# Performance work log

Measured on AMD Instinct MI355X. Metric: run time of the kernel, lower is better.

## Reference

```python
import jax, jax.numpy as jnp
import numpy as np

B, T, D, H = 8, 4096, 1024, 16
DK = D // H
CHUNK = 64
E, TOPK, MULT, CAPF = 8, 2, 4, 1.25
HID = D * MULT
N = B * T
CAPACITY = int(CAPF * (N / E))  # 5120


def setup_inputs() -> dict:
    key = jax.random.key(0)
    ks = jax.random.split(key, 16)
    s = 0.02
    r = lambda k, shape: jax.random.normal(k, shape, jnp.float32) * s
    return {
        "x": jax.random.normal(ks[0], (B, T, D), jnp.float32),
        "norm1_scale": jnp.ones((D,), jnp.float32),
        "norm2_scale": jnp.ones((D,), jnp.float32),
        "Wq": r(ks[1], (D, D)), "bq": jnp.zeros((D,), jnp.float32),
        "Wk": r(ks[2], (D, D)), "bk": jnp.zeros((D,), jnp.float32),
        "Wv": r(ks[3], (D, D)), "bv": jnp.zeros((D,), jnp.float32),
        "Wg": r(ks[4], (D, D)), "bg": jnp.zeros((D,), jnp.float32),
        "Wo": r(ks[5], (D, D)), "bo": jnp.zeros((D,), jnp.float32),
        "router_W": r(ks[6], (D, E)), "router_b": jnp.zeros((E,), jnp.float32),
        "W1": r(ks[7], (E, D, HID)), "b1": jnp.zeros((E, HID), jnp.float32),
        "W2": r(ks[8], (E, HID, D)), "b2": jnp.zeros((E, D), jnp.float32),
    }


def rmsnorm(x, scale):
    # torch: x / (||x|| / sqrt(d)) * scale == x * rsqrt(mean(x^2)) * scale (no eps)
    return x / jnp.sqrt(jnp.mean(x * x, axis=-1, keepdims=True)) * scale


def apply_rope(x):
    # x: (B, H, T, DK); non-interleaved half-rotation as in source
    half = x.shape[-1] // 2
    t = x.shape[2]
    inv = 1.0 / (10000.0 ** (jnp.arange(half, dtype=jnp.float32) / half))
    ang = jnp.arange(t, dtype=jnp.float32)[:, None] * inv[None, :]  # (T, half)
    sin, cos = jnp.sin(ang)[None, None], jnp.cos(ang)[None, None]
    x1, x2 = x[..., :half], x[..., half:]
    return jnp.concatenate([x1 * cos - x2 * sin, x1 * sin + x2 * cos], axis=-1)


def phi(x):
    return jax.nn.elu(x) + 1.0


def attention(x, Wq, bq, Wk, bk, Wv, bv, Wg, bg, Wo, bo):
    b, t, c = x.shape
    heads = lambda y: y.reshape(b, t, H, DK).transpose(0, 2, 1, 3)  # (B,H,T,DK)
    q = phi(apply_rope(heads(x @ Wq + bq)))
    k = phi(apply_rope(heads(x @ Wk + bk)))
    v = heads(x @ Wv + bv)
    g = heads(jax.nn.sigmoid(x @ Wg + bg))
    nc = t // CHUNK
    to_chunks = lambda y: y.reshape(b, H, nc, CHUNK, DK).transpose(2, 0, 1, 3, 4)
    qs, ks_, vs, gs = map(to_chunks, (q, k, v, g))  # (nc,B,H,chunk,DK)
    S0 = jnp.zeros((b, H, DK, DK), x.dtype)
    Z0 = jnp.zeros((b, H, DK), x.dtype)

    def step(carry, inp):
        S, Z = carry
        qc, kc, vc, gc = inp
        S = S + jnp.einsum('bhtd,bhte->bhde', kc, vc)
        Z = Z + kc.sum(axis=2)
        num = jnp.einsum('bhtd,bhde->bhte', qc, S)
        den = jnp.einsum('bhtd,bhd->bht', qc, Z)[..., None] + 1e-6
        return (S, Z), gc * (num / den)

    _, outs = jax.lax.scan(step, (S0, Z0), (qs, ks_, vs, gs))  # (nc,B,H,chunk,DK)
    out = outs.transpose(1, 2, 0, 3, 4).reshape(b, H, t, DK)
    out = out.transpose(0, 2, 1, 3).reshape(b, t, c)
    return out @ Wo + bo


def moe(x, router_W, router_b, W1, b1, W2, b2):
    b, t, c = x.shape
    n = b * t
    xf = x.reshape(n, c)
    probs = jax.nn.softmax(xf @ router_W + router_b, axis=-1)
    topk_probs, topk_idx = jax.lax.top_k(probs, TOPK)
    topk_probs = topk_probs / topk_probs.sum(axis=-1, keepdims=True)
    out = jnp.zeros_like(xf)
    load = []
    for eid in range(E):  # fixed small expert loop (matches source structure)
        mask = (topk_idx == eid).reshape(-1)  # row-major == torch.where order
        idx = jnp.nonzero(mask, size=CAPACITY, fill_value=n * TOPK)[0]
        valid = idx < n * TOPK
        idxc = jnp.minimum(idx, n * TOPK - 1)
        tok, choice = idxc // TOPK, idxc % TOPK
        h = jax.nn.gelu(xf[tok] @ W1[eid] + b1[eid], approximate=False) @ W2[eid] + b2[eid]
        gate = jnp.where(valid, topk_probs[tok, choice], 0.0)
        out = out.at[tok].add(gate[:, None] * h)  # invalid slots have gate==0
        load.append(jnp.minimum(mask.sum(), CAPACITY).astype(xf.dtype))
    load = jnp.stack(load)
    importance = probs.sum(axis=0)
    importance = importance / importance.sum()
    load = load / load.sum()
    aux = (importance * load).sum() * (E ** 2)
    return out.reshape(b, t, c), aux


def reference(x, norm1_scale, norm2_scale, Wq, bq, Wk, bk, Wv, bv, Wg, bg, Wo, bo,
              router_W, router_b, W1, b1, W2, b2):
    x = x + attention(rmsnorm(x, norm1_scale), Wq, bq, Wk, bk, Wv, bv, Wg, bg, Wo, bo)
    moe_out, aux = moe(rmsnorm(x, norm2_scale), router_W, router_b, W1, b1, W2, b2)
    return (x + moe_out, aux)
```

## Files before the change

kernel.cpp:

```cpp
#include <hip/hip_runtime.h>
#include <hip/hip_bf16.h>

#define NTOK 32768
#define TSEQ 4096
#define DM   1024
#define NHEAD 16
#define NEXP 8
#define CAPE 5120
#define HIDN 4096
#define GTOK 8192
#define KSPL 5120

#ifndef __has_builtin
#define __has_builtin(x) 0
#endif
#if __has_builtin(__builtin_amdgcn_global_load_lds)
#define HAVE_GLOAD 1
#else
#define HAVE_GLOAD 0
#endif

typedef __attribute__((ext_vector_type(8))) short bf16x8;
typedef __attribute__((ext_vector_type(4))) float f32x4;

// ... 135 lines not shown
    o.x = f2bf_bits(v.x * r * ns.x);
    o.y = f2bf_bits(v.y * r * ns.y);
    o.z = f2bf_bits(v.z * r * ns.z);
    o.w = f2bf_bits(v.w * r * ns.w);
    ((ushort4*)(xbf + (size_t)row * DM))[tid] = o;
}

#if HAVE_GLOAD
__device__ __forceinline__ void gload16(const __hip_bfloat16* g, __hip_bfloat16* l)
{
    __builtin_amdgcn_global_load_lds((const __attribute__((address_space(1))) unsigned int*)g,
                                     (__attribute__((address_space(3))) unsigned int*)l, 16, 0, 0);
}
#endif

struct ProjPack {
    const __hip_bfloat16* BT[4];
    const float* bias[4];
    float* C[4];
};

template<int NMAT, bool RESID>
__global__ __launch_bounds__(256) void k_gemm_proj(const __hip_bfloat16* __restrict__ A,
                                                   ProjPack P,
                                                   const float* __restrict__ resid)
{
    const int z = (NMAT == 4) ? blockIdx.z : 0;
    const __hip_bfloat16* BT = P.BT[z];
    const float* bias = P.bias[z];
    float* C = P.C[z];
    const int m0 = blockIdx.y * 128;
    const int n0 = blockIdx.x * 128;
    const int tid = threadIdx.x;
    __shared__ alignas(16) __hip_bfloat16 As[128 * 32];
    __shared__ alignas(16) __hip_bfloat16 Bs[128 * 32];

    const int lane = tid & 63, wv = tid >> 6;
    const int lr = lane & 15, lgp = lane >> 4;
    const int wm = (wv >> 1) * 64, wn = (wv & 1) * 64;

#if HAVE_GLOAD
    const int rA0 = wv * 32 + (lane >> 2), rA1 = rA0 + 16;
    const int ch = lane & 3;
    const __hip_bfloat16* srcA0 = A + (size_t)(m0 + rA0) * 3072 + ((ch ^ (rA0 & 3)) * 8);
    const __hip_bfloat16* srcA1 = A + (size_t)(m0 + rA1) * 3072 + ((ch ^ (rA1 & 3)) * 8);
    const __hip_bfloat16* srcB0 = BT + (size_t)(n0 + rA0) * KSPL + ((ch ^ (rA0 & 3)) * 8);
    const __hip_bfloat16* srcB1 = BT + (size_t)(n0 + rA1) * KSPL + ((ch ^ (rA1 & 3)) * 8);
    __hip_bfloat16* ldsA0 = As + (size_t)(wv * 32) * 32;
    __hip_bfloat16* ldsA1 = As + (size_t)(wv * 32 + 16) * 32;
    __hip_bfloat16* ldsB0 = Bs + (size_t)(wv * 32) * 32;
    __hip_bfloat16* ldsB1 = Bs + (size_t)(wv * 32 + 16) * 32;
#else
    const int ar = tid >> 1, ac0 = (tid & 1) * 2;
    const __hip_bfloat16* Arow = A + (size_t)(m0 + ar) * 3072;
    const __hip_bfloat16* Brow = BT + (size_t)(n0 + ar) * KSPL;
#endif

    f32x4 acc[4][4];
#pragma unroll
    for (int i = 0; i < 4; ++i)
#pragma unroll
        for (int j = 0; j < 4; ++j) acc[i][j] = (f32x4){0.f, 0.f, 0.f, 0.f};

    int a_off[4], b_off[4];
#pragma unroll
    for (int i = 0; i < 4; ++i) {
        int mrow = wm + i * 16 + lr;
        a_off[i] = mrow * 32 + ((lgp ^ (mrow & 3)) * 8);
        int nrow = wn + i * 16 + lr;
        b_off[i] = nrow * 32 + ((lgp ^ (nrow & 3)) * 8);
    }

    for (int k0 = 0; k0 < KSPL; k0 += 32) {
        const int acol = (k0 < 3072) ? k0 : (k0 - 3072);
        __syncthreads();
#if HAVE_GLOAD
        gload16(srcA0 + acol, ldsA0);
        gload16(srcA1 + acol, ldsA1);
        gload16(srcB0 + k0, ldsB0);
        gload16(srcB1 + k0, ldsB1);
#else
        {
            uint4 av0 = *(const uint4*)(Arow + acol + ac0 * 8);
            uint4 av1 = *(const uint4*)(Arow + acol + ac0 * 8 + 8);
            uint4 bv0 = *(const uint4*)(Brow + k0 + ac0 * 8);
            uint4 bv1 = *(const uint4*)(Brow + k0 + ac0 * 8 + 8);
            *(uint4*)(As + ar * 32 + ((ac0    ) ^ (ar & 3)) * 8) = av0;
            *(uint4*)(As + ar * 32 + ((ac0 + 1) ^ (ar & 3)) * 8) = av1;
            *(uint4*)(Bs + ar * 32 + ((ac0    ) ^ (ar & 3)) * 8) = bv0;
            *(uint4*)(Bs + ar * 32 + ((ac0 + 1) ^ (ar & 3)) * 8) = bv1;
        }
#endif
        __syncthreads();
        bf16x8 af[4], bfr[4];
#pragma unroll
        for (int i = 0; i < 4; ++i) af[i] = *(const bf16x8*)(As + a_off[i]);
#pragma unroll
        for (int j = 0; j < 4; ++j) bfr[j] = *(const bf16x8*)(Bs + b_off[j]);
#pragma unroll
        for (int i = 0; i < 4; ++i)
#pragma unroll
            for (int j = 0; j < 4; ++j)
                acc[i][j] = __builtin_amdgcn_mfma_f32_16x16x32_bf16(af[i], bfr[j], acc[i][j], 0, 0, 0);
    }

#pragma unroll
    for (int i = 0; i < 4; ++i)
#pragma unroll
        for (int j = 0; j < 4; ++j) {
            const int col = n0 + wn + j * 16 + lr;
            const float bval = bias[col];
#pragma unroll
            for (int r = 0; r < 4; ++r) {
                const int rloc = wm + i * 16 + lgp * 4 + r;
                float v = acc[i][j][r] + bval;
                if (RESID) v += resid[(size_t)(m0 + rloc) * DM + col];
                C[(size_t)(m0 + rloc) * DM + col] = v;
            }
        }
}

__global__ __launch_bounds__(256) void k_scan_kv(float* KS, float* Vz,
                                                 const float* __restrict__ ct,
                                                 const float* __restrict__ st)
{
    const int c = blockIdx.x, bh = blockIdx.y;
    const int h = bh & 15, b = bh >> 4;
    const int tid = threadIdx.x;
    __shared__ float ks[64][68];
    __shared__ float vs[64][68];
    const size_t rowbase = ((size_t)b * TSEQ + c * 64) * DM + h * 64;
#pragma unroll
    for (int p = 0; p < 8; ++p) {
        int idx = p * 256 + tid;
        int t = idx >> 5, j = idx & 31;
        const size_t base = rowbase + (size_t)t * DM + j;
        float cn = ct[(c * 64 + t) * 32 + j];
        float sn = st[(c * 64 + t) * 32 + j];
        float k1 = KS[base], k2 = KS[base + 32];
        ks[t][j]      = phi_f(k1 * cn - k2 * sn);
        ks[t][j + 32] = phi_f(k1 * sn + k2 * cn);
    }
#pragma unroll
    for (int p = 0; p < 4; ++p) {
        int idx = p * 256 + tid;
        int t = idx >> 4, e4 = (idx & 15) * 4;
        *(float4*)&vs[t][e4] = *(const float4*)&Vz[rowbase + (size_t)t * DM + e4];
    }
    __syncthreads();
    const int e = tid & 63, dg = tid >> 6;
    float acc[16] = {};
    for (int t = 0; t < 64; ++t) {
        float vv = vs[t][e];
#pragma unroll
        for (int q = 0; q < 4; ++q) {
            float4 kq = *(const float4*)&ks[t][dg * 16 + q * 4];
            acc[q * 4 + 0] = fmaf(kq.x, vv, acc[q * 4 + 0]);
            acc[q * 4 + 1] = fmaf(kq.y, vv, acc[q * 4 + 1]);
            acc[q * 4 + 2] = fmaf(kq.z, vv, acc[q * 4 + 2]);
            acc[q * 4 + 3] = fmaf(kq.w, vv, acc[q * 4 + 3]);
        }
    }
#pragma unroll
    for (int i = 0; i < 16; ++i) {
        int d = dg * 16 + i;
        KS[rowbase + (size_t)d * DM + e] = acc[i];
    }
    if (tid < 64) {
        float z = 0.f;
        for (int t = 0; t < 64; ++t) z += ks[t][tid];
        Vz[rowbase + tid] = z;
    }
}

__global__ __launch_bounds__(256) void k_scan_prefix(float* S)
{
    const int sg = blockIdx.x, bh = blockIdx.y;
    const int h = bh & 15, b = bh >> 4;
    const int idx = sg * 256 + threadIdx.x;
    const int d = idx >> 6, e = idx & 63;
    const size_t base = (size_t)b * TSEQ * DM + h * 64 + (size_t)d * DM + e;
    float acc = 0.f;
    for (int c = 0; c < 64; ++c) {
        size_t p = base + (size_t)c * 64 * DM;
        acc += S[p];
        S[p] = acc;
    }
}

__global__ void k_zprefix(float* Vz)
{
    const int bh = blockIdx.x;
    const int h = bh & 15, b = bh >> 4;
    const int d = threadIdx.x;
    const size_t base = (size_t)b * TSEQ * DM + h * 64 + d;
    float acc = 0.f;
    for (int c = 0; c < 64; ++c) {
        size_t p = base + (size_t)c * 64 * DM;
        acc += Vz[p];
        Vz[p] = acc;
    }
}

__global__ __launch_bounds__(256) void k_scan_out(const float* __restrict__ Q,
                                                  const float* __restrict__ S,
                                                  const float* __restrict__ Zv,
                                                  float* GO,
                                                  const float* __restrict__ ct,
                                                  const float* __restrict__ st)
{
    const int c = blockIdx.x, bh = blockIdx.y;
    const int h = bh & 15, b = bh >> 4;
    const int tid = threadIdx.x;
    __shared__ float qs[64][69];
    __shared__ float Ss[64][68];
    __shared__ float den[64], Zl[64];
    const size_t rowbase = ((size_t)b * TSEQ + c * 64) * DM + h * 64;
#pragma unroll
    for (int p = 0; p < 8; ++p) {
        int idx = p * 256 + tid;
        int t = idx >> 5, j = idx & 31;
        const size_t base = rowbase + (size_t)t * DM + j;
        float cn = ct[(c * 64 + t) * 32 + j];
        float sn = st[(c * 64 + t) * 32 + j];
        float q1 = Q[base], q2 = Q[base + 32];
        qs[t][j]      = phi_f(q1 * cn - q2 * sn);
        qs[t][j + 32] = phi_f(q1 * sn + q2 * cn);
    }
#pragma unroll
    for (int p = 0; p < 4; ++p) {
        int idx = p * 256 + tid;
        int d = idx >> 4, e4 = (idx & 15) * 4;
        *(float4*)&Ss[d][e4] = *(const float4*)&S[rowbase + (size_t)d * DM + e4];
    }
    const int e = tid & 63, tg = tid >> 6;
    float greg[16];
#pragma unroll
    for (int i = 0; i < 16; ++i)
        greg[i] = GO[rowbase + (size_t)(tg * 16 + i) * DM + e];
    if (tid < 64) Zl[tid] = Zv[rowbase + tid];
    __syncthreads();
    if (tid < 64) {
        float dd = 0.f;
        for (int d = 0; d < 64; ++d) dd += qs[tid][d] * Zl[d];
        den[tid] = dd + 1e-6f;
    }
    __syncthreads();
    float acc[16] = {};
    for (int d = 0; d < 64; ++d) {
        float sv = Ss[d][e];
#pragma unroll
        for (int i = 0; i < 16; ++i)
            acc[i] = fmaf(qs[tg * 16 + i][d], sv, acc[i]);
    }
#pragma unroll
    for (int i = 0; i < 16; ++i) {
        int t = tg * 16 + i;
        float g = 1.f / (1.f + expf(-greg[i]));
        GO[rowbase + (size_t)t * DM + e] = g * acc[i] / den[t];
    }
}

__global__ __launch_bounds__(256) void k_router(const float* __restrict__ X2,
                                                const float* __restrict__ rn2,
                                                const float* __restrict__ ns2,
                                                const float* __restrict__ rW,
                                                const float* __restrict__ rb,
                                                int* __restrict__ route_e,
                                                float* __restrict__ route_g,
                                                float* __restrict__ probs)
{
    const int tok = blockIdx.x * 4 + (threadIdx.x >> 6);
    const int lane = threadIdx.x & 63;
    const float* xr = X2 + (size_t)tok * DM;
    const float rn = rn2[tok];
    float lg[8] = {};
    for (int d = lane; d < DM; d += 64) {
        float xv = xr[d] * rn * ns2[d];
        const float4* w4 = (const float4*)(rW + (size_t)d * 8);
        float4 w0 = w4[0], w1 = w4[1];
        lg[0] += xv * w0.x; lg[1] += xv * w0.y; lg[2] += xv * w0.z; lg[3] += xv * w0.w;
        lg[4] += xv * w1.x; lg[5] += xv * w1.y; lg[6] += xv * w1.z; lg[7] += xv * w1.w;
    }
#pragma unroll
    for (int e = 0; e < 8; ++e)
        for (int off = 32; off; off >>= 1) lg[e] += __shfl_xor(lg[e], off);
    if (lane == 0) {
        float pe[8]; float mx = -1e30f, s = 0.f;
#pragma unroll
        for (int e = 0; e < 8; ++e) { lg[e] += rb[e]; mx = fmaxf(mx, lg[e]); }
#pragma unroll
        for (int e = 0; e < 8; ++e) { pe[e] = expf(lg[e] - mx); s += pe[e]; }
#pragma unroll
        for (int e = 0; e < 8; ++e) { pe[e] /= s; probs[(size_t)tok * 8 + e] = pe[e]; }
        int i1 = 0; float p1 = pe[0];
#pragma unroll
        for (int e = 1; e < 8; ++e) if (pe[e] > p1) { p1 = pe[e]; i1 = e; }
        int i2 = -1; float p2 = -1.f;
#pragma unroll
        for (int e = 0; e < 8; ++e) if (e != i1 && pe[e] > p2) { p2 = pe[e]; i2 = e; }
        const float gsum = p1 + p2;
        route_e[tok * 2] = i1; route_e[tok * 2 + 1] = i2;
        route_g[tok * 2] = p1 / gsum; route_g[tok * 2 + 1] = p2 / gsum;
    }
}

__global__ __launch_bounds__(256) void k_count(const int* __restrict__ route_e, int* __restrict__ bcnt)
{
    __shared__ int c[8];
    const int tid = threadIdx.x;
    if (tid < 8) c[tid] = 0;
    __syncthreads();
    atomicAdd(&c[route_e[blockIdx.x * 256 + tid]], 1);
    __syncthreads();
    if (tid < 8) bcnt[blockIdx.x * 8 + tid] = c[tid];
}

__global__ void k_scan_blocks(const int* __restrict__ bcnt, int* __restrict__ bbase, int* __restrict__ ctot)
{
    const int e = threadIdx.x;
    if (e < 8) {
        int run = 0;
        for (int b = 0; b < 256; ++b) { bbase[b * 8 + e] = run; run += bcnt[b * 8 + e]; }
        ctot[e] = run;
    }
}

__global__ __launch_bounds__(256) void k_place(const int* __restrict__ route_e,
                                               const float* __restrict__ route_g,
                                               const int* __restrict__ bbase,
                                               int* __restrict__ tokslot,
                                               float* __restrict__ gateslot)
{
    const int tid = threadIdx.x;
    const int a = blockIdx.x * 256 + tid;
    const int e = route_e[a];
    __shared__ int se[256];
    se[tid] = e;
    __syncthreads();
    int rank = 0;
    for (int j = 0; j < tid; ++j) rank += (se[j] == e) ? 1 : 0;
    const int slot = bbase[blockIdx.x * 8 + e] + rank;
    if (slot < CAPE) {
        tokslot[e * CAPE + slot] = a >> 1;
        gateslot[e * CAPE + slot] = route_g[a];
    }
}

__global__ __launch_bounds__(256) void k_aux(const float* __restrict__ probs,
                                             const int* __restrict__ ctot,
                                             float* __restrict__ out_aux)
{
    const int tid = threadIdx.x;
    float part[8] = {};
    for (int i = tid; i < NTOK; i += 256) {
        const float* p = probs + (size_t)i * 8;
#pragma unroll
        for (int e = 0; e < 8; ++e) part[e] += p[e];
    }
    __shared__ float red[256];
    __shared__ float accs[8];
    for (int e = 0; e < 8; ++e) {
        red[tid] = part[e];
        __syncthreads();
        for (int s = 128; s; s >>= 1) { if (tid < s) red[tid] += red[tid + s]; __syncthreads(); }
        if (tid == 0) accs[e] = red[0];
        __syncthreads();
    }
    if (tid == 0) {
        float isum = 0.f, lsum = 0.f, l[8];
        for (int e = 0; e < 8; ++e) isum += accs[e];
        for (int e = 0; e < 8; ++e) { l[e] = fminf((float)ctot[e], (float)CAPE); lsum += l[e]; }
        float aux = 0.f;
        for (int e = 0; e < 8; ++e) aux += (accs[e] / isum) * (l[e] / lsum);
        out_aux[0] = aux * 64.f;
    }
}

__global__ void k_transpose_bf16(const float* __restrict__ src, __hip_bfloat16* __restrict__ dst,
                                 int K_, int N_)
{
    __shared__ float t_[32][33];
    const int z = blockIdx.z;
    const float* s = src + (size_t)z * K_ * N_;
    __hip_bfloat16* d = dst + (size_t)z * K_ * N_;
    const int n0 = blockIdx.x * 32, k0 = blockIdx.y * 32;
    const int c = threadIdx.x, r0 = threadIdx.y;
#pragma unroll
    for (int i = 0; i < 4; ++i) { int r = r0 + i * 8; t_[r][c] = s[(size_t)(k0 + r) * N_ + n0 + c]; }
    __syncthreads();
#pragma unroll
    for (int i = 0; i < 4; ++i) { int r = r0 + i * 8; d[(size_t)(n0 + r) * K_ + k0 + c] = __float2bfloat16(t_[c][r]); }
}

template<int MODE>
__global__ __launch_bounds__(256) void k_gemm_bf16(const __hip_bfloat16* __restrict__ A,
                                                   const __hip_bfloat16* __restrict__ BT,
                                                   const float* __restrict__ bias,
                                                   __hip_bfloat16* __restrict__ Hout,
                                                   float* __restrict__ Fout,
                                                   const int* __restrict__ tokslot,
                                                   const float* __restrict__ gateslot,
                                                   int K, int Nout, int e0)
{
    const int le = blockIdx.z;
    const int e = e0 + le;
    const int m0 = blockIdx.y * 128;
    const int n0 = blockIdx.x * 128;
    const int tid = threadIdx.x;
    __shared__ alignas(16) __hip_bfloat16 As[128 * 32];
    __shared__ alignas(16) __hip_bfloat16 Bs[128 * 32];
    __shared__ int s_tok[128];
    __shared__ float s_gate[128];
    if (tid < 128) {
        s_tok[tid] = tokslot[e * CAPE + m0 + tid];
        s_gate[tid] = gateslot[e * CAPE + m0 + tid];
    }
    __syncthreads();

    const int lane = tid & 63, wv = tid >> 6;
    const int lr = lane & 15, lgp = lane >> 4;
    const int wm = (wv >> 1) * 64, wn = (wv & 1) * 64;

#if HAVE_GLOAD
    const int rA0 = wv * 32 + (lane >> 2), rA1 = rA0 + 16;
    const int ch = lane & 3;
    const __hip_bfloat16 *srcA0, *srcA1;
    if (MODE == 0) {
        srcA0 = A + (size_t)s_tok[rA0] * K + ((ch ^ (rA0 & 3)) * 8);
        srcA1 = A + (size_t)s_tok[rA1] * K + ((ch ^ (rA1 & 3)) * 8);
    } else {
        srcA0 = A + ((size_t)le * CAPE + m0 + rA0) * K + ((ch ^ (rA0 & 3)) * 8);
        srcA1 = A + ((size_t)le * CAPE + m0 + rA1) * K + ((ch ^ (rA1 & 3)) * 8);
    }
    const __hip_bfloat16* srcB0 = BT + ((size_t)e * Nout + n0 + rA0) * K + ((ch ^ (rA0 & 3)) * 8);
    const __hip_bfloat16* srcB1 = BT + ((size_t)e * Nout + n0 + rA1) * K + ((ch ^ (rA1 & 3)) * 8);
    __hip_bfloat16* ldsA0 = As + (size_t)(wv * 32) * 32;
    __hip_bfloat16* ldsA1 = As + (size_t)(wv * 32 + 16) * 32;
    __hip_bfloat16* ldsB0 = Bs + (size_t)(wv * 32) * 32;
    __hip_bfloat16* ldsB1 = Bs + (size_t)(wv * 32 + 16) * 32;
#else
    const int ar = tid >> 1, ac0 = (tid & 1) * 2;
    const __hip_bfloat16* Arow;
    if (MODE == 0) Arow = A + (size_t)s_tok[ar] * K;
    else           Arow = A + ((size_t)le * CAPE + m0 + ar) * K;
    const __hip_bfloat16* Brow = BT + ((size_t)e * Nout + n0 + ar) * K;
#endif

    f32x4 acc[4][4];
#pragma unroll
    for (int i = 0; i < 4; ++i)
#pragma unroll
        for (int j = 0; j < 4; ++j) acc[i][j] = (f32x4){0.f, 0.f, 0.f, 0.f};

    int a_off[4], b_off[4];
#pragma unroll
    for (int i = 0; i < 4; ++i) {
        int mrow = wm + i * 16 + lr;
        a_off[i] = mrow * 32 + ((lgp ^ (mrow & 3)) * 8);
        int nrow = wn + i * 16 + lr;
        b_off[i] = nrow * 32 + ((lgp ^ (nrow & 3)) * 8);
    }

    for (int k0 = 0; k0 < K; k0 += 32) {
        __syncthreads();
#if HAVE_GLOAD
        gload16(srcA0 + k0, ldsA0);
        gload16(srcA1 + k0, ldsA1);
        gload16(srcB0 + k0, ldsB0);
        gload16(srcB1 + k0, ldsB1);
#else
        {
            uint4 av0 = *(const uint4*)(Arow + k0 + ac0 * 8);
            uint4 av1 = *(const uint4*)(Arow + k0 + ac0 * 8 + 8);
            uint4 bv0 = *(const uint4*)(Brow + k0 + ac0 * 8);
            uint4 bv1 = *(const uint4*)(Brow + k0 + ac0 * 8 + 8);
            *(uint4*)(As + ar * 32 + ((ac0    ) ^ (ar & 3)) * 8) = av0;
            *(uint4*)(As + ar * 32 + ((ac0 + 1) ^ (ar & 3)) * 8) = av1;
            *(uint4*)(Bs + ar * 32 + ((ac0    ) ^ (ar & 3)) * 8) = bv0;
            *(uint4*)(Bs + ar * 32 + ((ac0 + 1) ^ (ar & 3)) * 8) = bv1;
        }
#endif
        __syncthreads();
        bf16x8 af[4], bfr[4];
#pragma unroll
        for (int i = 0; i < 4; ++i) af[i] = *(const bf16x8*)(As + a_off[i]);
#pragma unroll
        for (int j = 0; j < 4; ++j) bfr[j] = *(const bf16x8*)(Bs + b_off[j]);
#pragma unroll
        for (int i = 0; i < 4; ++i)
#pragma unroll
            for (int j = 0; j < 4; ++j)
                acc[i][j] = __builtin_amdgcn_mfma_f32_16x16x32_bf16(af[i], bfr[j], acc[i][j], 0, 0, 0);
    }

#pragma unroll
    for (int i = 0; i < 4; ++i)
#pragma unroll
        for (int j = 0; j < 4; ++j) {
            const int col = n0 + wn + j * 16 + lr;
            const float bval = bias[(size_t)e * Nout + col];
#pragma unroll
            for (int r = 0; r < 4; ++r) {
                const int rloc = wm + i * 16 + lgp * 4 + r;
                float v = acc[i][j][r] + bval;
                if (MODE == 0) {
                    v = 0.5f * v * (1.f + erff(v * 0.70710678118654752f));
                    Hout[((size_t)le * CAPE + m0 + rloc) * Nout + col] = __float2bfloat16(v);
                } else {
                    const float g = s_gate[rloc];
                    if (g != 0.f) atomicAdd(&Fout[(size_t)s_tok[rloc] * DM + col], v * g);
                }
            }
        }
}

extern "C" void kernel_launch(void* const* d_in, const int* in_sizes, int n_in,
                              void* d_out, int out_size, void* d_ws, size_t ws_size,
                              hipStream_t stream)
{
    (void)in_sizes; (void)n_in; (void)out_size;
    const float* x   = (const float*)d_in[0];
    const float* ns1 = (const float*)d_in[1];
    const float* ns2 = (const float*)d_in[2];
    const float* Wq  = (const float*)d_in[3];
    const float* bq  = (const float*)d_in[4];
    const float* Wk  = (const float*)d_in[5];
    const float* bk  = (const float*)d_in[6];
    const float* Wv  = (const float*)d_in[7];
// ... 64 lines not shown
        const float* xg = x + tok0 * DM;
        float* vg = out + tok0 * DM;

        k_rms_split<true><<<GTOK, 256, 0, stream>>>(xg, ns1, Xs);

        ProjPack P;
        P.BT[0] = WST;                     P.bias[0] = bq; P.C[0] = qg;
        P.BT[1] = WST + (size_t)DM * KSPL; P.bias[1] = bk; P.C[1] = kg;
        P.BT[2] = WST + 2ull * DM * KSPL;  P.bias[2] = bg; P.C[2] = gg;
        P.BT[3] = WST + 3ull * DM * KSPL;  P.bias[3] = bv; P.C[3] = vg;
        k_gemm_proj<4, false><<<dim3(8, GTOK / 128, 4), 256, 0, stream>>>(Xs, P, nullptr);

        k_scan_kv<<<dim3(64, 32), 256, 0, stream>>>(kg, vg, rope_ct, rope_st);
        k_scan_prefix<<<dim3(16, 32), 256, 0, stream>>>(kg);
        k_zprefix<<<32, 64, 0, stream>>>(vg);
        k_scan_out<<<dim3(64, 32), 256, 0, stream>>>(qg, kg, vg, gg, rope_ct, rope_st);

        k_rms_split<false><<<GTOK, 256, 0, stream>>>(gg, nullptr, Xs);

        ProjPack P2;
        P2.BT[0] = WST + 4ull * DM * KSPL; P2.bias[0] = bo; P2.C[0] = vg;
        P2.BT[1] = P2.BT[2] = P2.BT[3] = P2.BT[0];
        P2.bias[1] = P2.bias[2] = P2.bias[3] = bo;
        P2.C[1] = P2.C[2] = P2.C[3] = vg;
        k_gemm_proj<1, true><<<dim3(8, GTOK / 128, 1), 256, 0, stream>>>(Xs, P2, xg);

        k_rmsnorm_stats<<<GTOK, 256, 0, stream>>>(vg, rn2 + tok0, ns2, xn2bf + tok0 * DM);
    }

    k_router<<<NTOK / 4, 256, 0, stream>>>(out, rn2, ns2, rW, rb, route_e, route_g, probs);

    k_count<<<256, 256, 0, stream>>>(route_e, bcnt);
    k_scan_blocks<<<1, 64, 0, stream>>>(bcnt, bbase, ctot);
// ... 18 lines not shown
```

Before: 4.618 ms.

## Double-buffer LDS in GEMM kernels and fuse bf16 split into scan output

Both the projection GEMM and the expert GEMM now use two LDS buffers per operand. The next K-slice is prefetched into the spare buffer while MFMAs run on the current one, leaving one barrier per iteration instead of two. The scan output kernel now writes the three-way bf16 split directly into the GEMM input buffer, which removes the separate k_rms_split pass over the gated output. The cost is double the LDS per block, which may lower occupancy.

```diff
diff --git a/kernel.cpp b/kernel.cpp
--- a/kernel.cpp
+++ b/kernel.cpp
@@ -173,6 +173,7 @@
 }
 #endif
 
+
 struct ProjPack {
     const __hip_bfloat16* BT[4];
     const float* bias[4];
@@ -191,8 +192,8 @@
     const int m0 = blockIdx.y * 128;
     const int n0 = blockIdx.x * 128;
     const int tid = threadIdx.x;
-    __shared__ alignas(16) __hip_bfloat16 As[128 * 32];
-    __shared__ alignas(16) __hip_bfloat16 Bs[128 * 32];
+    __shared__ alignas(16) __hip_bfloat16 As[2][128 * 32];
+    __shared__ alignas(16) __hip_bfloat16 Bs[2][128 * 32];
 
     const int lane = tid & 63, wv = tid >> 6;
     const int lr = lane & 15, lgp = lane >> 4;
@@ -205,10 +206,8 @@
     const __hip_bfloat16* srcA1 = A + (size_t)(m0 + rA1) * 3072 + ((ch ^ (rA1 & 3)) * 8);
     const __hip_bfloat16* srcB0 = BT + (size_t)(n0 + rA0) * KSPL + ((ch ^ (rA0 & 3)) * 8);
     const __hip_bfloat16* srcB1 = BT + (size_t)(n0 + rA1) * KSPL + ((ch ^ (rA1 & 3)) * 8);
-    __hip_bfloat16* ldsA0 = As + (size_t)(wv * 32) * 32;
-    __hip_bfloat16* ldsA1 = As + (size_t)(wv * 32 + 16) * 32;
-    __hip_bfloat16* ldsB0 = Bs + (size_t)(wv * 32) * 32;
-    __hip_bfloat16* ldsB1 = Bs + (size_t)(wv * 32 + 16) * 32;
+    const int ldsO0 = (wv * 32) * 32;
+    const int ldsO1 = (wv * 32 + 16) * 32;
 #else
     const int ar = tid >> 1, ac0 = (tid & 1) * 2;
     const __hip_bfloat16* Arow = A + (size_t)(m0 + ar) * 3072;
@@ -230,37 +229,58 @@
         b_off[i] = nrow * 32 + ((lgp ^ (nrow & 3)) * 8);
     }
 
+#if HAVE_GLOAD
+    gload16(srcA0, &As[0][ldsO0]);
+    gload16(srcA1, &As[0][ldsO1]);
+    gload16(srcB0, &Bs[0][ldsO0]);
+    gload16(srcB1, &Bs[0][ldsO1]);
+#else
+    {
+        uint4 av0 = *(const uint4*)(Arow + ac0 * 8);
+        uint4 av1 = *(const uint4*)(Arow + ac0 * 8 + 8);
+        uint4 bv0 = *(const uint4*)(Brow + ac0 * 8);
+        uint4 bv1 = *(const uint4*)(Brow + ac0 * 8 + 8);
+        *(uint4*)(&As[0][0] + ar * 32 + ((ac0    ) ^ (ar & 3)) * 8) = av0;
+        *(uint4*)(&As[0][0] + ar * 32 + ((ac0 + 1) ^ (ar & 3)) * 8) = av1;
+        *(uint4*)(&Bs[0][0] + ar * 32 + ((ac0    ) ^ (ar & 3)) * 8) = bv0;
+        *(uint4*)(&Bs[0][0] + ar * 32 + ((ac0 + 1) ^ (ar & 3)) * 8) = bv1;
+    }
+#endif
+    __syncthreads();
+
+    int cur = 0;
     for (int k0 = 0; k0 < KSPL; k0 += 32) {
-        const int acol = (k0 < 3072) ? k0 : (k0 - 3072);
-        __syncthreads();
+        if (k0 + 32 < KSPL) {
+            const int kn = k0 + 32;
+            const int acoln = (kn < 3072) ? kn : (kn - 3072);
 #if HAVE_GLOAD
-        gload16(srcA0 + acol, ldsA0);
-        gload16(srcA1 + acol, ldsA1);
-        gload16(srcB0 + k0, ldsB0);
-        gload16(srcB1 + k0, ldsB1);
+            gload16(srcA0 + acoln, &As[cur ^ 1][ldsO0]);
+            gload16(srcA1 + acoln, &As[cur ^ 1][ldsO1]);
+            gload16(srcB0 + kn, &Bs[cur ^ 1][ldsO0]);
+            gload16(srcB1 + kn, &Bs[cur ^ 1][ldsO1]);
 #else
-        {
-            uint4 av0 = *(const uint4*)(Arow + acol + ac0 * 8);
-            uint4 av1 = *(const uint4*)(Arow + acol + ac0 * 8 + 8);
-            uint4 bv0 = *(const uint4*)(Brow + k0 + ac0 * 8);
-            uint4 bv1 = *(const uint4*)(Brow + k0 + ac0 * 8 + 8);
-            *(uint4*)(As + ar * 32 + ((ac0    ) ^ (ar & 3)) * 8) = av0;
-            *(uint4*)(As + ar * 32 + ((ac0 + 1) ^ (ar & 3)) * 8) = av1;
-            *(uint4*)(Bs + ar * 32 + ((ac0    ) ^ (ar & 3)) * 8) = bv0;
-            *(uint4*)(Bs + ar * 32 + ((ac0 + 1) ^ (ar & 3)) * 8) = bv1;
+            uint4 av0 = *(const uint4*)(Arow + acoln + ac0 * 8);
+            uint4 av1 = *(const uint4*)(Arow + acoln + ac0 * 8 + 8);
+            uint4 bv0 = *(const uint4*)(Brow + kn + ac0 * 8);
+            uint4 bv1 = *(const uint4*)(Brow + kn + ac0 * 8 + 8);
+            *(uint4*)(&As[cur ^ 1][0] + ar * 32 + ((ac0    ) ^ (ar & 3)) * 8) = av0;
+            *(uint4*)(&As[cur ^ 1][0] + ar * 32 + ((ac0 + 1) ^ (ar & 3)) * 8) = av1;
+            *(uint4*)(&Bs[cur ^ 1][0] + ar * 32 + ((ac0    ) ^ (ar & 3)) * 8) = bv0;
+            *(uint4*)(&Bs[cur ^ 1][0] + ar * 32 + ((ac0 + 1) ^ (ar & 3)) * 8) = bv1;
+#endif
         }
-#endif
-        __syncthreads();
         bf16x8 af[4], bfr[4];
 #pragma unroll
-        for (int i = 0; i < 4; ++i) af[i] = *(const bf16x8*)(As + a_off[i]);
-#pragma unroll
-        for (int j = 0; j < 4; ++j) bfr[j] = *(const bf16x8*)(Bs + b_off[j]);
+        for (int i = 0; i < 4; ++i) af[i] = *(const bf16x8*)(&As[cur][0] + a_off[i]);
+#pragma unroll
+        for (int j = 0; j < 4; ++j) bfr[j] = *(const bf16x8*)(&Bs[cur][0] + b_off[j]);
 #pragma unroll
         for (int i = 0; i < 4; ++i)
 #pragma unroll
             for (int j = 0; j < 4; ++j)
                 acc[i][j] = __builtin_amdgcn_mfma_f32_16x16x32_bf16(af[i], bfr[j], acc[i][j], 0, 0, 0);
+        __syncthreads();
+        cur ^= 1;
     }
 
 #pragma unroll
@@ -277,279 +297,6 @@
                 C[(size_t)(m0 + rloc) * DM + col] = v;
             }
         }
-}
-
-__global__ __launch_bounds__(256) void k_scan_kv(float* KS, float* Vz,
-                                                 const float* __restrict__ ct,
-                                                 const float* __restrict__ st)
-{
-    const int c = blockIdx.x, bh = blockIdx.y;
-    const int h = bh & 15, b = bh >> 4;
-    const int tid = threadIdx.x;
-    __shared__ float ks[64][68];
-    __shared__ float vs[64][68];
-    const size_t rowbase = ((size_t)b * TSEQ + c * 64) * DM + h * 64;
-#pragma unroll
-    for (int p = 0; p < 8; ++p) {
-        int idx = p * 256 + tid;
-        int t = idx >> 5, j = idx & 31;
-        const size_t base = rowbase + (size_t)t * DM + j;
-        float cn = ct[(c * 64 + t) * 32 + j];
-        float sn = st[(c * 64 + t) * 32 + j];
-        float k1 = KS[base], k2 = KS[base + 32];
-        ks[t][j]      = phi_f(k1 * cn - k2 * sn);
-        ks[t][j + 32] = phi_f(k1 * sn + k2 * cn);
-    }
-#pragma unroll
-    for (int p = 0; p < 4; ++p) {
-        int idx = p * 256 + tid;
-        int t = idx >> 4, e4 = (idx & 15) * 4;
-        *(float4*)&vs[t][e4] = *(const float4*)&Vz[rowbase + (size_t)t * DM + e4];
-    }
-    __syncthreads();
-    const int e = tid & 63, dg = tid >> 6;
-    float acc[16] = {};
-    for (int t = 0; t < 64; ++t) {
-        float vv = vs[t][e];
-#pragma unroll
-        for (int q = 0; q < 4; ++q) {
-            float4 kq = *(const float4*)&ks[t][dg * 16 + q * 4];
-            acc[q * 4 + 0] = fmaf(kq.x, vv, acc[q * 4 + 0]);
-            acc[q * 4 + 1] = fmaf(kq.y, vv, acc[q * 4 + 1]);
-            acc[q * 4 + 2] = fmaf(kq.z, vv, acc[q * 4 + 2]);
-            acc[q * 4 + 3] = fmaf(kq.w, vv, acc[q * 4 + 3]);
-        }
-    }
-#pragma unroll
-    for (int i = 0; i < 16; ++i) {
-        int d = dg * 16 + i;
-        KS[rowbase + (size_t)d * DM + e] = acc[i];
-    }
-    if (tid < 64) {
-        float z = 0.f;
-        for (int t = 0; t < 64; ++t) z += ks[t][tid];
-        Vz[rowbase + tid] = z;
-    }
-}
-
-__global__ __launch_bounds__(256) void k_scan_prefix(float* S)
-{
-    const int sg = blockIdx.x, bh = blockIdx.y;
-    const int h = bh & 15, b = bh >> 4;
-    const int idx = sg * 256 + threadIdx.x;
-    const int d = idx >> 6, e = idx & 63;
-    const size_t base = (size_t)b * TSEQ * DM + h * 64 + (size_t)d * DM + e;
-    float acc = 0.f;
-    for (int c = 0; c < 64; ++c) {
-        size_t p = base + (size_t)c * 64 * DM;
-        acc += S[p];
-        S[p] = acc;
-    }
-}
-
-__global__ void k_zprefix(float* Vz)
-{
-    const int bh = blockIdx.x;
-    const int h = bh & 15, b = bh >> 4;
-    const int d = threadIdx.x;
-    const size_t base = (size_t)b * TSEQ * DM + h * 64 + d;
-    float acc = 0.f;
-    for (int c = 0; c < 64; ++c) {
-        size_t p = base + (size_t)c * 64 * DM;
-        acc += Vz[p];
-        Vz[p] = acc;
-    }
-}
-
-__global__ __launch_bounds__(256) void k_scan_out(const float* __restrict__ Q,
-                                                  const float* __restrict__ S,
-                                                  const float* __restrict__ Zv,
-                                                  float* GO,
-                                                  const float* __restrict__ ct,
-                                                  const float* __restrict__ st)
-{
-    const int c = blockIdx.x, bh = blockIdx.y;
-    const int h = bh & 15, b = bh >> 4;
-    const int tid = threadIdx.x;
-    __shared__ float qs[64][69];
-    __shared__ float Ss[64][68];
-    __shared__ float den[64], Zl[64];
-    const size_t rowbase = ((size_t)b * TSEQ + c * 64) * DM + h * 64;
-#pragma unroll
-    for (int p = 0; p < 8; ++p) {
-        int idx = p * 256 + tid;
-        int t = idx >> 5, j = idx & 31;
-        const size_t base = rowbase + (size_t)t * DM + j;
-        float cn = ct[(c * 64 + t) * 32 + j];
-        float sn = st[(c * 64 + t) * 32 + j];
-        float q1 = Q[base], q2 = Q[base + 32];
-        qs[t][j]      = phi_f(q1 * cn - q2 * sn);
-        qs[t][j + 32] = phi_f(q1 * sn + q2 * cn);
-    }
-#pragma unroll
-    for (int p = 0; p < 4; ++p) {
-        int idx = p * 256 + tid;
-        int d = idx >> 4, e4 = (idx & 15) * 4;
-        *(float4*)&Ss[d][e4] = *(const float4*)&S[rowbase + (size_t)d * DM + e4];
-    }
-    const int e = tid & 63, tg = tid >> 6;
-    float greg[16];
-#pragma unroll
-    for (int i = 0; i < 16; ++i)
-        greg[i] = GO[rowbase + (size_t)(tg * 16 + i) * DM + e];
-    if (tid < 64) Zl[tid] = Zv[rowbase + tid];
-    __syncthreads();
-    if (tid < 64) {
-        float dd = 0.f;
-        for (int d = 0; d < 64; ++d) dd += qs[tid][d] * Zl[d];
-        den[tid] = dd + 1e-6f;
-    }
-    __syncthreads();
-    float acc[16] = {};
-    for (int d = 0; d < 64; ++d) {
-        float sv = Ss[d][e];
-#pragma unroll
-        for (int i = 0; i < 16; ++i)
-            acc[i] = fmaf(qs[tg * 16 + i][d], sv, acc[i]);
-    }
-#pragma unroll
-    for (int i = 0; i < 16; ++i) {
-        int t = tg * 16 + i;
-        float g = 1.f / (1.f + expf(-greg[i]));
-        GO[rowbase + (size_t)t * DM + e] = g * acc[i] / den[t];
-    }
-}
-
-__global__ __launch_bounds__(256) void k_router(const float* __restrict__ X2,
-                                                const float* __restrict__ rn2,
-                                                const float* __restrict__ ns2,
-                                                const float* __restrict__ rW,
-                                                const float* __restrict__ rb,
-                                                int* __restrict__ route_e,
-                                                float* __restrict__ route_g,
-                                                float* __restrict__ probs)
-{
-    const int tok = blockIdx.x * 4 + (threadIdx.x >> 6);
-    const int lane = threadIdx.x & 63;
-    const float* xr = X2 + (size_t)tok * DM;
-    const float rn = rn2[tok];
-    float lg[8] = {};
-    for (int d = lane; d < DM; d += 64) {
-        float xv = xr[d] * rn * ns2[d];
-        const float4* w4 = (const float4*)(rW + (size_t)d * 8);
-        float4 w0 = w4[0], w1 = w4[1];
-        lg[0] += xv * w0.x; lg[1] += xv * w0.y; lg[2] += xv * w0.z; lg[3] += xv * w0.w;
-        lg[4] += xv * w1.x; lg[5] += xv * w1.y; lg[6] += xv * w1.z; lg[7] += xv * w1.w;
-    }
-#pragma unroll
-    for (int e = 0; e < 8; ++e)
-        for (int off = 32; off; off >>= 1) lg[e] += __shfl_xor(lg[e], off);
-    if (lane == 0) {
-        float pe[8]; float mx = -1e30f, s = 0.f;
-#pragma unroll
-        for (int e = 0; e < 8; ++e) { lg[e] += rb[e]; mx = fmaxf(mx, lg[e]); }
-#pragma unroll
-        for (int e = 0; e < 8; ++e) { pe[e] = expf(lg[e] - mx); s += pe[e]; }
-#pragma unroll
-        for (int e = 0; e < 8; ++e) { pe[e] /= s; probs[(size_t)tok * 8 + e] = pe[e]; }
-        int i1 = 0; float p1 = pe[0];
-#pragma unroll
-        for (int e = 1; e < 8; ++e) if (pe[e] > p1) { p1 = pe[e]; i1 = e; }
-        int i2 = -1; float p2 = -1.f;
-#pragma unroll
-        for (int e = 0; e < 8; ++e) if (e != i1 && pe[e] > p2) { p2 = pe[e]; i2 = e; }
-        const float gsum = p1 + p2;
-        route_e[tok * 2] = i1; route_e[tok * 2 + 1] = i2;
-        route_g[tok * 2] = p1 / gsum; route_g[tok * 2 + 1] = p2 / gsum;
-    }
-}
-
-__global__ __launch_bounds__(256) void k_count(const int* __restrict__ route_e, int* __restrict__ bcnt)
-{
-    __shared__ int c[8];
-    const int tid = threadIdx.x;
-    if (tid < 8) c[tid] = 0;
-    __syncthreads();
-    atomicAdd(&c[route_e[blockIdx.x * 256 + tid]], 1);
-    __syncthreads();
-    if (tid < 8) bcnt[blockIdx.x * 8 + tid] = c[tid];
-}
-
-__global__ void k_scan_blocks(const int* __restrict__ bcnt, int* __restrict__ bbase, int* __restrict__ ctot)
-{
-    const int e = threadIdx.x;
-    if (e < 8) {
-        int run = 0;
-        for (int b = 0; b < 256; ++b) { bbase[b * 8 + e] = run; run += bcnt[b * 8 + e]; }
-        ctot[e] = run;
-    }
-}
-
-__global__ __launch_bounds__(256) void k_place(const int* __restrict__ route_e,
-                                               const float* __restrict__ route_g,
-                                               const int* __restrict__ bbase,
-                                               int* __restrict__ tokslot,
-                                               float* __restrict__ gateslot)
-{
-    const int tid = threadIdx.x;
-    const int a = blockIdx.x * 256 + tid;
-    const int e = route_e[a];
-    __shared__ int se[256];
-    se[tid] = e;
-    __syncthreads();
-    int rank = 0;
-    for (int j = 0; j < tid; ++j) rank += (se[j] == e) ? 1 : 0;
-    const int slot = bbase[blockIdx.x * 8 + e] + rank;
-    if (slot < CAPE) {
-        tokslot[e * CAPE + slot] = a >> 1;
-        gateslot[e * CAPE + slot] = route_g[a];
-    }
-}
-
-__global__ __launch_bounds__(256) void k_aux(const float* __restrict__ probs,
-                                             const int* __restrict__ ctot,
-                                             float* __restrict__ out_aux)
-{
-    const int tid = threadIdx.x;
-    float part[8] = {};
-    for (int i = tid; i < NTOK; i += 256) {
-        const float* p = probs + (size_t)i * 8;
-#pragma unroll
-        for (int e = 0; e < 8; ++e) part[e] += p[e];
-    }
-    __shared__ float red[256];
-    __shared__ float accs[8];
-    for (int e = 0; e < 8; ++e) {
-        red[tid] = part[e];
-        __syncthreads();
-        for (int s = 128; s; s >>= 1) { if (tid < s) red[tid] += red[tid + s]; __syncthreads(); }
-        if (tid == 0) accs[e] = red[0];
-        __syncthreads();
-    }
-    if (tid == 0) {
-        float isum = 0.f, lsum = 0.f, l[8];
-        for (int e = 0; e < 8; ++e) isum += accs[e];
-        for (int e = 0; e < 8; ++e) { l[e] = fminf((float)ctot[e], (float)CAPE); lsum += l[e]; }
-        float aux = 0.f;
-        for (int e = 0; e < 8; ++e) aux += (accs[e] / isum) * (l[e] / lsum);
-        out_aux[0] = aux * 64.f;
-    }
-}
-
-__global__ void k_transpose_bf16(const float* __restrict__ src, __hip_bfloat16* __restrict__ dst,
-                                 int K_, int N_)
-{
-    __shared__ float t_[32][33];
-    const int z = blockIdx.z;
-    const float* s = src + (size_t)z * K_ * N_;
-    __hip_bfloat16* d = dst + (size_t)z * K_ * N_;
-    const int n0 = blockIdx.x * 32, k0 = blockIdx.y * 32;
-    const int c = threadIdx.x, r0 = threadIdx.y;
-#pragma unroll
-    for (int i = 0; i < 4; ++i) { int r = r0 + i * 8; t_[r][c] = s[(size_t)(k0 + r) * N_ + n0 + c]; }
-    __syncthreads();
-#pragma unroll
-    for (int i = 0; i < 4; ++i) { int r = r0 + i * 8; d[(size_t)(n0 + r) * K_ + k0 + c] = __float2bfloat16(t_[c][r]); }
 }
 
 template<int MODE>
@@ -567,8 +314,8 @@
     const int m0 = blockIdx.y * 128;
     const int n0 = blockIdx.x * 128;
     const int tid = threadIdx.x;
-    __shared__ alignas(16) __hip_bfloat16 As[128 * 32];
-    __shared__ alignas(16) __hip_bfloat16 Bs[128 * 32];
+    __shared__ alignas(16) __hip_bfloat16 As[2][128 * 32];
+    __shared__ alignas(16) __hip_bfloat16 Bs[2][128 * 32];
     __shared__ int s_tok[128];
     __shared__ float s_gate[128];
     if (tid < 128) {
@@ -594,10 +341,8 @@
     }
     const __hip_bfloat16* srcB0 = BT + ((size_t)e * Nout + n0 + rA0) * K + ((ch ^ (rA0 & 3)) * 8);
     const __hip_bfloat16* srcB1 = BT + ((size_t)e * Nout + n0 + rA1) * K + ((ch ^ (rA1 & 3)) * 8);
-    __hip_bfloat16* ldsA0 = As + (size_t)(wv * 32) * 32;
-    __hip_bfloat16* ldsA1 = As + (size_t)(wv * 32 + 16) * 32;
-    __hip_bfloat16* ldsB0 = Bs + (size_t)(wv * 32) * 32;
-    __hip_bfloat16* ldsB1 = Bs + (size_t)(wv * 32 + 16) * 32;
+    const int ldsO0 = (wv * 32) * 32;
+    const int ldsO1 = (wv * 32 + 16) * 32;
 #else
     const int ar = tid >> 1, ac0 = (tid & 1) * 2;
     const __hip_bfloat16* Arow;
@@ -621,36 +366,57 @@
         b_off[i] = nrow * 32 + ((lgp ^ (nrow & 3)) * 8);
     }
 
+#if HAVE_GLOAD
+    gload16(srcA0, &As[0][ldsO0]);
+    gload16(srcA1, &As[0][ldsO1]);
+    gload16(srcB0, &Bs[0][ldsO0]);
+    gload16(srcB1, &Bs[0][ldsO1]);
+#else
+    {
+        uint4 av0 = *(const uint4*)(Arow + ac0 * 8);
+        uint4 av1 = *(const uint4*)(Arow + ac0 * 8 + 8);
+        uint4 bv0 = *(const uint4*)(Brow + ac0 * 8);
+        uint4 bv1 = *(const uint4*)(Brow + ac0 * 8 + 8);
+        *(uint4*)(&As[0][0] + ar * 32 + ((ac0    ) ^ (ar & 3)) * 8) = av0;
+        *(uint4*)(&As[0][0] + ar * 32 + ((ac0 + 1) ^ (ar & 3)) * 8) = av1;
+        *(uint4*)(&Bs[0][0] + ar * 32 + ((ac0    ) ^ (ar & 3)) * 8) = bv0;
+        *(uint4*)(&Bs[0][0] + ar * 32 + ((ac0 + 1) ^ (ar & 3)) * 8) = bv1;
+    }
+#endif
+    __syncthreads();
+
+    int cur = 0;
     for (int k0 = 0; k0 < K; k0 += 32) {
-        __syncthreads();
+        if (k0 + 32 < K) {
+            const int kn = k0 + 32;
 #if HAVE_GLOAD
-        gload16(srcA0 + k0, ldsA0);
-        gload16(srcA1 + k0, ldsA1);
-        gload16(srcB0 + k0, ldsB0);
-        gload16(srcB1 + k0, ldsB1);
+            gload16(srcA0 + kn, &As[cur ^ 1][ldsO0]);
+            gload16(srcA1 + kn, &As[cur ^ 1][ldsO1]);
+            gload16(srcB0 + kn, &Bs[cur ^ 1][ldsO0]);
+            gload16(srcB1 + kn, &Bs[cur ^ 1][ldsO1]);
 #else
-        {
-            uint4 av0 = *(const uint4*)(Arow + k0 + ac0 * 8);
-            uint4 av1 = *(const uint4*)(Arow + k0 + ac0 * 8 + 8);
-            uint4 bv0 = *(const uint4*)(Brow + k0 + ac0 * 8);
-            uint4 bv1 = *(const uint4*)(Brow + k0 + ac0 * 8 + 8);
-            *(uint4*)(As + ar * 32 + ((ac0    ) ^ (ar & 3)) * 8) = av0;
-            *(uint4*)(As + ar * 32 + ((ac0 + 1) ^ (ar & 3)) * 8) = av1;
-            *(uint4*)(Bs + ar * 32 + ((ac0    ) ^ (ar & 3)) * 8) = bv0;
-            *(uint4*)(Bs + ar * 32 + ((ac0 + 1) ^ (ar & 3)) * 8) = bv1;
+            uint4 av0 = *(const uint4*)(Arow + kn + ac0 * 8);
+            uint4 av1 = *(const uint4*)(Arow + kn + ac0 * 8 + 8);
+            uint4 bv0 = *(const uint4*)(Brow + kn + ac0 * 8);
+            uint4 bv1 = *(const uint4*)(Brow + kn + ac0 * 8 + 8);
+            *(uint4*)(&As[cur ^ 1][0] + ar * 32 + ((ac0    ) ^ (ar & 3)) * 8) = av0;
+            *(uint4*)(&As[cur ^ 1][0] + ar * 32 + ((ac0 + 1) ^ (ar & 3)) * 8) = av1;
+            *(uint4*)(&Bs[cur ^ 1][0] + ar * 32 + ((ac0    ) ^ (ar & 3)) * 8) = bv0;
+            *(uint4*)(&Bs[cur ^ 1][0] + ar * 32 + ((ac0 + 1) ^ (ar & 3)) * 8) = bv1;
+#endif
         }
-#endif
-        __syncthreads();
         bf16x8 af[4], bfr[4];
 #pragma unroll
-        for (int i = 0; i < 4; ++i) af[i] = *(const bf16x8*)(As + a_off[i]);
-#pragma unroll
-        for (int j = 0; j < 4; ++j) bfr[j] = *(const bf16x8*)(Bs + b_off[j]);
+        for (int i = 0; i < 4; ++i) af[i] = *(const bf16x8*)(&As[cur][0] + a_off[i]);
+#pragma unroll
+        for (int j = 0; j < 4; ++j) bfr[j] = *(const bf16x8*)(&Bs[cur][0] + b_off[j]);
 #pragma unroll
         for (int i = 0; i < 4; ++i)
 #pragma unroll
             for (int j = 0; j < 4; ++j)
                 acc[i][j] = __builtin_amdgcn_mfma_f32_16x16x32_bf16(af[i], bfr[j], acc[i][j], 0, 0, 0);
+        __syncthreads();
+        cur ^= 1;
     }
 
 #pragma unroll
@@ -672,6 +438,290 @@
                 }
             }
         }
+}
+
+__global__ __launch_bounds__(256) void k_scan_kv(float* KS, float* Vz,
+                                                 const float* __restrict__ ct,
+                                                 const float* __restrict__ st)
+{
+    const int c = blockIdx.x, bh = blockIdx.y;
+    const int h = bh & 15, b = bh >> 4;
+    const int tid = threadIdx.x;
+    __shared__ float ks[64][68];
+    __shared__ float vs[64][68];
+    const size_t rowbase = ((size_t)b * TSEQ + c * 64) * DM + h * 64;
+#pragma unroll
+    for (int p = 0; p < 8; ++p) {
+        int idx = p * 256 + tid;
+        int t = idx >> 5, j = idx & 31;
+        const size_t base = rowbase + (size_t)t * DM + j;
+        float cn = ct[(c * 64 + t) * 32 + j];
+        float sn = st[(c * 64 + t) * 32 + j];
+        float k1 = KS[base], k2 = KS[base + 32];
+        ks[t][j]      = phi_f(k1 * cn - k2 * sn);
+        ks[t][j + 32] = phi_f(k1 * sn + k2 * cn);
+    }
+#pragma unroll
+    for (int p = 0; p < 4; ++p) {
+        int idx = p * 256 + tid;
+        int t = idx >> 4, e4 = (idx & 15) * 4;
+        *(float4*)&vs[t][e4] = *(const float4*)&Vz[rowbase + (size_t)t * DM + e4];
+    }
+    __syncthreads();
+    const int e = tid & 63, dg = tid >> 6;
+    float acc[16] = {};
+    for (int t = 0; t < 64; ++t) {
+        float vv = vs[t][e];
+#pragma unroll
+        for (int qq = 0; qq < 4; ++qq) {
+            float4 kq = *(const float4*)&ks[t][dg * 16 + qq * 4];
+            acc[qq * 4 + 0] = fmaf(kq.x, vv, acc[qq * 4 + 0]);
+            acc[qq * 4 + 1] = fmaf(kq.y, vv, acc[qq * 4 + 1]);
+            acc[qq * 4 + 2] = fmaf(kq.z, vv, acc[qq * 4 + 2]);
+            acc[qq * 4 + 3] = fmaf(kq.w, vv, acc[qq * 4 + 3]);
+        }
+    }
+#pragma unroll
+    for (int i = 0; i < 16; ++i) {
+        int d = dg * 16 + i;
+        KS[rowbase + (size_t)d * DM + e] = acc[i];
+    }
+    if (tid < 64) {
+        float z = 0.f;
+        for (int t = 0; t < 64; ++t) z += ks[t][tid];
+        Vz[rowbase + tid] = z;
+    }
+}
+
+__global__ __launch_bounds__(256) void k_scan_prefix(float* S)
+{
+    const int sg = blockIdx.x, bh = blockIdx.y;
+    const int h = bh & 15, b = bh >> 4;
+    const int idx = sg * 256 + threadIdx.x;
+    const int d = idx >> 6, e = idx & 63;
+    const size_t base = (size_t)b * TSEQ * DM + h * 64 + (size_t)d * DM + e;
+    float acc = 0.f;
+    for (int c = 0; c < 64; ++c) {
+        size_t p = base + (size_t)c * 64 * DM;
+        acc += S[p];
+        S[p] = acc;
+    }
+}
+
+__global__ void k_zprefix(float* Vz)
+{
+    const int bh = blockIdx.x;
+    const int h = bh & 15, b = bh >> 4;
+    const int d = threadIdx.x;
+    const size_t base = (size_t)b * TSEQ * DM + h * 64 + d;
+    float acc = 0.f;
+    for (int c = 0; c < 64; ++c) {
+        size_t p = base + (size_t)c * 64 * DM;
+        acc += Vz[p];
+        Vz[p] = acc;
+    }
+}
+
+__global__ __launch_bounds__(256) void k_scan_out(const float* __restrict__ Q,
+                                                  const float* __restrict__ S,
+                                                  const float* __restrict__ Zv,
+                                                  const float* __restrict__ G,
+                                                  __hip_bfloat16* __restrict__ Xs,
+                                                  const float* __restrict__ ct,
+                                                  const float* __restrict__ st)
+{
+    const int c = blockIdx.x, bh = blockIdx.y;
+    const int h = bh & 15, b = bh >> 4;
+    const int tid = threadIdx.x;
+    __shared__ float qs[64][69];
+    __shared__ float Ss[64][68];
+    __shared__ float den[64], Zl[64];
+    const size_t rowbase = ((size_t)b * TSEQ + c * 64) * DM + h * 64;
+#pragma unroll
+    for (int p = 0; p < 8; ++p) {
+        int idx = p * 256 + tid;
+        int t = idx >> 5, j = idx & 31;
+        const size_t base = rowbase + (size_t)t * DM + j;
+        float cn = ct[(c * 64 + t) * 32 + j];
+        float sn = st[(c * 64 + t) * 32 + j];
+        float q1 = Q[base], q2 = Q[base + 32];
+        qs[t][j]      = phi_f(q1 * cn - q2 * sn);
+        qs[t][j + 32] = phi_f(q1 * sn + q2 * cn);
+    }
+#pragma unroll
+    for (int p = 0; p < 4; ++p) {
+        int idx = p * 256 + tid;
+        int d = idx >> 4, e4 = (idx & 15) * 4;
+        *(float4*)&Ss[d][e4] = *(const float4*)&S[rowbase + (size_t)d * DM + e4];
+    }
+    const int e = tid & 63, tg = tid >> 6;
+    float greg[16];
+#pragma unroll
+    for (int i = 0; i < 16; ++i)
+        greg[i] = G[rowbase + (size_t)(tg * 16 + i) * DM + e];
+    if (tid < 64) Zl[tid] = Zv[rowbase + tid];
+    __syncthreads();
+    if (tid < 64) {
+        float dd = 0.f;
+        for (int d = 0; d < 64; ++d) dd += qs[tid][d] * Zl[d];
+        den[tid] = dd + 1e-6f;
+    }
+    __syncthreads();
+    float acc[16] = {};
+    for (int d = 0; d < 64; ++d) {
+        float sv = Ss[d][e];
+#pragma unroll
+        for (int i = 0; i < 16; ++i)
+            acc[i] = fmaf(qs[tg * 16 + i][d], sv, acc[i]);
+    }
+    unsigned short* Xu = (unsigned short*)Xs;
+#pragma unroll
+    for (int i = 0; i < 16; ++i) {
+        int t = tg * 16 + i;
+        float g = 1.f / (1.f + expf(-greg[i]));
+        float o = g * acc[i] / den[t];
+        unsigned short b0 = f2bf_bits(o);
+        float r1 = o - bf_to_f(b0);
+        unsigned short b1 = f2bf_bits(r1);
+        float r2 = r1 - bf_to_f(b1);
+        unsigned short b2 = f2bf_bits(r2);
+        const size_t xb = (size_t)(b * TSEQ + c * 64 + t) * 3072 + h * 64 + e;
+        Xu[xb] = b0;
+        Xu[xb + 1024] = b1;
+        Xu[xb + 2048] = b2;
+    }
+}
+
+__global__ __launch_bounds__(256) void k_router(const float* __restrict__ X2,
+                                                const float* __restrict__ rn2,
+                                                const float* __restrict__ ns2,
+                                                const float* __restrict__ rW,
+                                                const float* __restrict__ rb,
+                                                int* __restrict__ route_e,
+                                                float* __restrict__ route_g,
+                                                float* __restrict__ probs)
+{
+    const int tok = blockIdx.x * 4 + (threadIdx.x >> 6);
+    const int lane = threadIdx.x & 63;
+    const float* xr = X2 + (size_t)tok * DM;
+    const float rn = rn2[tok];
+    float lg[8] = {};
+    for (int d = lane; d < DM; d += 64) {
+        float xv = xr[d] * rn * ns2[d];
+        const float4* w4 = (const float4*)(rW + (size_t)d * 8);
+        float4 w0 = w4[0], w1 = w4[1];
+        lg[0] += xv * w0.x; lg[1] += xv * w0.y; lg[2] += xv * w0.z; lg[3] += xv * w0.w;
+        lg[4] += xv * w1.x; lg[5] += xv * w1.y; lg[6] += xv * w1.z; lg[7] += xv * w1.w;
+    }
+#pragma unroll
+    for (int e = 0; e < 8; ++e)
+        for (int off = 32; off; off >>= 1) lg[e] += __shfl_xor(lg[e], off);
+    if (lane == 0) {
+        float pe[8]; float mx = -1e30f, s = 0.f;
+#pragma unroll
+        for (int e = 0; e < 8; ++e) { lg[e] += rb[e]; mx = fmaxf(mx, lg[e]); }
+#pragma unroll
+        for (int e = 0; e < 8; ++e) { pe[e] = expf(lg[e] - mx); s += pe[e]; }
+#pragma unroll
+        for (int e = 0; e < 8; ++e) { pe[e] /= s; probs[(size_t)tok * 8 + e] = pe[e]; }
+        int i1 = 0; float p1 = pe[0];
+#pragma unroll
+        for (int e = 1; e < 8; ++e) if (pe[e] > p1) { p1 = pe[e]; i1 = e; }
+        int i2 = -1; float p2 = -1.f;
+#pragma unroll
+        for (int e = 0; e < 8; ++e) if (e != i1 && pe[e] > p2) { p2 = pe[e]; i2 = e; }
+        const float gsum = p1 + p2;
+        route_e[tok * 2] = i1; route_e[tok * 2 + 1] = i2;
+        route_g[tok * 2] = p1 / gsum; route_g[tok * 2 + 1] = p2 / gsum;
+    }
+}
+
+__global__ __launch_bounds__(256) void k_count(const int* __restrict__ route_e, int* __restrict__ bcnt)
+{
+    __shared__ int c[8];
+    const int tid = threadIdx.x;
+    if (tid < 8) c[tid] = 0;
+    __syncthreads();
+    atomicAdd(&c[route_e[blockIdx.x * 256 + tid]], 1);
+    __syncthreads();
+    if (tid < 8) bcnt[blockIdx.x * 8 + tid] = c[tid];
+}
+
+__global__ void k_scan_blocks(const int* __restrict__ bcnt, int* __restrict__ bbase, int* __restrict__ ctot)
+{
+    const int e = threadIdx.x;
+    if (e < 8) {
+        int run = 0;
+        for (int b = 0; b < 256; ++b) { bbase[b * 8 + e] = run; run += bcnt[b * 8 + e]; }
+        ctot[e] = run;
+    }
+}
+
+__global__ __launch_bounds__(256) void k_place(const int* __restrict__ route_e,
+                                               const float* __restrict__ route_g,
+                                               const int* __restrict__ bbase,
+                                               int* __restrict__ tokslot,
+                                               float* __restrict__ gateslot)
+{
+    const int tid = threadIdx.x;
+    const int a = blockIdx.x * 256 + tid;
+    const int e = route_e[a];
+    __shared__ int se[256];
+    se[tid] = e;
+    __syncthreads();
+    int rank = 0;
+    for (int j = 0; j < tid; ++j) rank += (se[j] == e) ? 1 : 0;
+    const int slot = bbase[blockIdx.x * 8 + e] + rank;
+    if (slot < CAPE) {
+        tokslot[e * CAPE + slot] = a >> 1;
+        gateslot[e * CAPE + slot] = route_g[a];
+    }
+}
+
+__global__ __launch_bounds__(256) void k_aux(const float* __restrict__ probs,
+                                             const int* __restrict__ ctot,
+                                             float* __restrict__ out_aux)
+{
+    const int tid = threadIdx.x;
+    float part[8] = {};
+    for (int i = tid; i < NTOK; i += 256) {
+        const float* p = probs + (size_t)i * 8;
+#pragma unroll
+        for (int e = 0; e < 8; ++e) part[e] += p[e];
+    }
+    __shared__ float red[256];
+    __shared__ float accs[8];
+    for (int e = 0; e < 8; ++e) {
+        red[tid] = part[e];
+        __syncthreads();
+        for (int s = 128; s; s >>= 1) { if (tid < s) red[tid] += red[tid + s]; __syncthreads(); }
+        if (tid == 0) accs[e] = red[0];
+        __syncthreads();
+    }
+    if (tid == 0) {
+        float isum = 0.f, lsum = 0.f, l[8];
+        for (int e = 0; e < 8; ++e) isum += accs[e];
+        for (int e = 0; e < 8; ++e) { l[e] = fminf((float)ctot[e], (float)CAPE); lsum += l[e]; }
+        float aux = 0.f;
+        for (int e = 0; e < 8; ++e) aux += (accs[e] / isum) * (l[e] / lsum);
+        out_aux[0] = aux * 64.f;
+    }
+}
+
+__global__ void k_transpose_bf16(const float* __restrict__ src, __hip_bfloat16* __restrict__ dst,
+                                 int K_, int N_)
+{
+    __shared__ float t_[32][33];
+    const int z = blockIdx.z;
+    const float* s = src + (size_t)z * K_ * N_;
+    __hip_bfloat16* d = dst + (size_t)z * K_ * N_;
+    const int n0 = blockIdx.x * 32, k0 = blockIdx.y * 32;
+    const int c = threadIdx.x, r0 = threadIdx.y;
+#pragma unroll
+    for (int i = 0; i < 4; ++i) { int r = r0 + i * 8; t_[r][c] = s[(size_t)(k0 + r) * N_ + n0 + c]; }
+    __syncthreads();
+#pragma unroll
+    for (int i = 0; i < 4; ++i) { int r = r0 + i * 8; d[(size_t)(n0 + r) * K_ + k0 + c] = __float2bfloat16(t_[c][r]); }
 }
 
 extern "C" void kernel_launch(void* const* d_in, const int* in_sizes, int n_in,
@@ -766,9 +816,7 @@
         k_scan_kv<<<dim3(64, 32), 256, 0, stream>>>(kg, vg, rope_ct, rope_st);
         k_scan_prefix<<<dim3(16, 32), 256, 0, stream>>>(kg);
         k_zprefix<<<32, 64, 0, stream>>>(vg);
-        k_scan_out<<<dim3(64, 32), 256, 0, stream>>>(qg, kg, vg, gg, rope_ct, rope_st);
-
-        k_rms_split<false><<<GTOK, 256, 0, stream>>>(gg, nullptr, Xs);
+        k_scan_out<<<dim3(64, 32), 256, 0, stream>>>(qg, kg, vg, gg, Xs, rope_ct, rope_st);
 
         ProjPack P2;
         P2.BT[0] = WST + 4ull * DM * KSPL; P2.bias[0] = bo; P2.C[0] = vg;
```

Measured after the change: 4.610 ms. Within noise of the previous version (-0.2%).
